# Kernel optimization log

Measured on AMD Instinct MI355X. Metric: run time of the kernel, lower is better.

## Reference

```python
import jax, jax.numpy as jnp
import numpy as np

HEAD_SIZE = 64


def setup_inputs() -> dict:
    key = jax.random.key(0)
    k1, k2, k3, k4 = jax.random.split(key, 4)
    B, T, E = 8, 2048, 1024
    x = jax.random.normal(k1, (B, T, E), dtype=jnp.float32)
    # nn.Linear(n_embd, head_size, bias=False) weights: [head_size, n_embd]
    s = 1.0 / np.sqrt(E)
    Wk = jax.random.uniform(k2, (HEAD_SIZE, E), jnp.float32, -s, s)
    Wq = jax.random.uniform(k3, (HEAD_SIZE, E), jnp.float32, -s, s)
    Wv = jax.random.uniform(k4, (HEAD_SIZE, E), jnp.float32, -s, s)
    return {"x": x, "Wk": Wk, "Wq": Wq, "Wv": Wv}


def reference(x, Wk, Wq, Wv):
    # x: [B, T, E]; W*: [D, E] with D = head_size
    B, T, E = x.shape
    k = jnp.einsum("bte,de->btd", x, Wk)  # [B,T,D]
    q = jnp.einsum("bte,de->btd", x, Wq)
    v = jnp.einsum("bte,de->btd", x, Wv)
    scale = k.shape[-1] ** -0.5
    wei = jnp.einsum("btd,bsd->bts", q, k) * scale  # [B,T,T]
    causal = jnp.tril(jnp.ones((T, T), dtype=bool))
    wei = jnp.where(causal, wei, -jnp.inf)
    wei = jax.nn.softmax(wei, axis=-1)
    # dropout p=0.0 (eval): identity
    return jnp.einsum("bts,bsd->btd", wei, v)
```

## Files before the change

### kernel.cpp

```cpp
#include <hip/hip_runtime.h>
#include <hip/hip_bf16.h>


typedef __bf16 bf16x8 __attribute__((ext_vector_type(8)));
typedef float  f32x4  __attribute__((ext_vector_type(4)));

#define T_SEQ 2048
#define E_DIM 1024
#define D_HEAD 64
#define M_TOT 16384
#define NSPLIT 4
#define SC_LOG2E 0.18033688011112042f

__device__ __forceinline__ unsigned short f2b(float f) {
  union { float f; unsigned int u; } cv; cv.f = f;
  unsigned int u = cv.u;
  u += 0x7FFFu + ((u >> 16) & 1u);
  return (unsigned short)(u >> 16);
}

__device__ __forceinline__ unsigned int f2b2(float a, float b) {
#if __has_builtin(__builtin_amdgcn_cvt_pk_bf16_f32)
  typedef __bf16 bf16x2_t __attribute__((ext_vector_type(2)));
  union { bf16x2_t v; unsigned int u; } cv;
  cv.v = __builtin_amdgcn_cvt_pk_bf16_f32(a, b);
  return cv.u;
#else
  return (unsigned int)f2b(a) | ((unsigned int)f2b(b) << 16);
#endif
}

__device__ __forceinline__ void dma16(const unsigned short* g, unsigned short* l) {
  __builtin_amdgcn_global_load_lds(
      (const __attribute__((address_space(1))) void*)g,
      (__attribute__((address_space(3))) void*)l, 16, 0, 0);
}

__global__ __launch_bounds__(256) void wcvt_kernel(
    const float* __restrict__ Wk, const float* __restrict__ Wq,
    const float* __restrict__ Wv, unsigned short* __restrict__ Wb)
{
  int i = blockIdx.x * 256 + threadIdx.x;
  int n = i >> 8, c4 = i & 255;
  const float* src = (n < 64) ? Wq + n * E_DIM
                   : (n < 128) ? Wk + (n - 64) * E_DIM
                               : Wv + (n - 128) * E_DIM;
  float4 v = *(const float4*)(src + c4 * 4);
  *(uint2*)(Wb + (size_t)n * E_DIM + c4 * 4) = make_uint2(f2b2(v.x, v.y), f2b2(v.z, v.w));
}

__global__ __launch_bounds__(256, 2) void proj_kernel(
    const float* __restrict__ x, const unsigned short* __restrict__ Wb,
    unsigned short* __restrict__ qws, unsigned short* __restrict__ kws,
    unsigned short* __restrict__ vtws)
{
  __shared__ __align__(16) unsigned short x_lds[2][32 * 64];
  __shared__ __align__(16) unsigned short w_lds[2][192 * 64];

  const int tid = threadIdx.x, wv = tid >> 6, lane = tid & 63;
  const int c = lane & 15, quad = lane >> 4;
  const int row0 = blockIdx.x * 32;

  const int f0r = tid >> 4, f0c = tid & 15;
  const int f1r = 16 + f0r;
  const float* xp0 = x + (size_t)(row0 + f0r) * E_DIM + f0c * 4;
  const float* xp1 = x + (size_t)(row0 + f1r) * E_DIM + f0c * 4;
  const int xa0 = f0r * 64 + (((f0c >> 1) ^ (f0r & 7)) << 3) + (f0c & 1) * 4;
  const int xa1 = f1r * 64 + (((f0c >> 1) ^ (f1r & 7)) << 3) + (f0c & 1) * 4;

  auto stageW = [&](int k0, int buf) {
    for (int j = 0; j < 6; ++j) {
      int base_r = (wv * 6 + j) * 8;
      int r = base_r + (lane >> 3);
      int g = (lane & 7) ^ (r & 7);
      dma16(Wb + (size_t)r * E_DIM + k0 + g * 8, &w_lds[buf][base_r * 64]);
    }
  };
  auto writeX = [&](float4 v0, float4 v1, int buf) {
    *(uint2*)&x_lds[buf][xa0] = make_uint2(f2b2(v0.x, v0.y), f2b2(v0.z, v0.w));
    *(uint2*)&x_lds[buf][xa1] = make_uint2(f2b2(v1.x, v1.y), f2b2(v1.z, v1.w));
  };

  f32x4 acc[6];
  for (int j = 0; j < 6; ++j)
    for (int r = 0; r < 4; ++r) acc[j][r] = 0.0f;

  stageW(0, 0);
  {
    float4 v0 = *(const float4*)xp0;
    float4 v1 = *(const float4*)xp1;
    writeX(v0, v1, 0);
  }

  for (int s = 0; s < 16; ++s) {
    const int cur = s & 1;
    __syncthreads();
    float4 v0, v1;
    if (s < 15) {
      const int k1 = (s + 1) * 64;
      stageW(k1, cur ^ 1);
      v0 = *(const float4*)(xp0 + k1);
      v1 = *(const float4*)(xp1 + k1);
    }
    for (int ks = 0; ks < 2; ++ks) {
      const int pg = ((ks * 4 + quad) ^ (c & 7)) << 3;
      bf16x8 a0 = *(const bf16x8*)&x_lds[cur][c * 64 + pg];
      bf16x8 a1 = *(const bf16x8*)&x_lds[cur][(16 + c) * 64 + pg];
      for (int j = 0; j < 3; ++j) {
        const int n = (wv * 3 + j) * 16 + c;
        bf16x8 bb = *(const bf16x8*)&w_lds[cur][n * 64 + pg];
        acc[j * 2]     = __builtin_amdgcn_mfma_f32_16x16x32_bf16(a0, bb, acc[j * 2], 0, 0, 0);
        acc[j * 2 + 1] = __builtin_amdgcn_mfma_f32_16x16x32_bf16(a1, bb, acc[j * 2 + 1], 0, 0, 0);
      }
    }
    if (s < 15) writeX(v0, v1, cur ^ 1);
  }

  for (int mt = 0; mt < 2; ++mt) {
    const int rbase = row0 + mt * 16 + quad * 4;
    for (int j = 0; j < 3; ++j) {
      const int nt = wv * 3 + j;
      const f32x4 a = acc[j * 2 + mt];
      if (nt < 4) {
        int d = nt * 16 + c;
        for (int r = 0; r < 4; ++r)
          qws[(size_t)(rbase + r) * D_HEAD + d] = f2b(a[r] * SC_LOG2E);
      } else if (nt < 8) {
        int d = (nt - 4) * 16 + c;
        for (int r = 0; r < 4; ++r)
          kws[(size_t)(rbase + r) * D_HEAD + d] = f2b(a[r]);
      } else {
        int d = (nt - 8) * 16 + c;
        int bb = rbase >> 11, tt = rbase & 2047;
        *(ushort4*)&vtws[(size_t)bb * D_HEAD * T_SEQ + (size_t)d * T_SEQ + tt] =
            make_ushort4(f2b(a[0]), f2b(a[1]), f2b(a[2]), f2b(a[3]));
      }
    }
  }
}

__global__ __launch_bounds__(256, 4) void attn_kernel(
    const unsigned short* __restrict__ qws, const unsigned short* __restrict__ kws,
    const unsigned short* __restrict__ vtws,
    unsigned short* __restrict__ opart, float* __restrict__ lpart)
{
  __shared__ __align__(16) unsigned short k_lds[2 * 64 * 64];
  __shared__ __align__(16) unsigned short v_lds[2 * 64 * 64];
  __shared__ __align__(16) unsigned short p_lds[64 * 64];

  const int tid = threadIdx.x, wv = tid >> 6, lane = tid & 63;
  const int c = lane & 15, quad = lane >> 4;
  const int qt = blockIdx.x, b = blockIdx.y, sg = blockIdx.z;
  const int t0 = qt * 64;
  const size_t qkb = (size_t)b * T_SEQ * D_HEAD;
  const size_t vtb = (size_t)b * D_HEAD * T_SEQ;
  const int niter = (qt >= sg) ? ((qt - sg) >> 2) + 1 : 0;
  const int rloc = wv * 16 + quad * 4;
  const size_t prow = ((size_t)sg * 8 + b) * T_SEQ;

  if (niter == 0) {
    for (int nt = 0; nt < 4; ++nt)
      for (int r = 0; r < 4; ++r)
        opart[(prow + t0 + rloc + r) * D_HEAD + nt * 16 + c] = 0;
    if (c == 0)
      for (int r = 0; r < 4; ++r) lpart[prow + t0 + rloc + r] = 0.0f;
    return;
  }

  const int mrow = wv * 16 + c;
  const bf16x8 qf0 = *(const bf16x8*)(qws + qkb + (size_t)(t0 + mrow) * D_HEAD + quad * 8);
  const bf16x8 qf1 = *(const bf16x8*)(qws + qkb + (size_t)(t0 + mrow) * D_HEAD + 32 + quad * 8);

  bf16x8 ones;
  { union { unsigned short s[8]; bf16x8 v; } o;
    for (int i = 0; i < 8; ++i) o.s[i] = 0x3F80;
    ones = o.v; }

  f32x4 acc_o[4], acc_l;
  for (int r = 0; r < 4; ++r) acc_l[r] = 0.0f;
  for (int nt = 0; nt < 4; ++nt)
    for (int r = 0; r < 4; ++r) acc_o[nt][r] = 0.0f;

  auto stageKV = [&](int s0, int buf) {
    unsigned short* kb = k_lds + buf * 4096;
    unsigned short* vb = v_lds + buf * 4096;
    for (int j = 0; j < 2; ++j) {
      int base = (wv * 2 + j) * 64;
      int p = base + lane;
      int r = p >> 3, g = (p & 7) ^ (r & 7);
      dma16(kws + qkb + (size_t)(s0 + r) * D_HEAD + g * 8, kb + base * 8);
    }
    for (int j = 0; j < 2; ++j) {
      int base = (wv * 2 + j) * 64;
      int p = base + lane;
      int r = p >> 3, g = (p & 7) ^ (r & 7);
      dma16(vtws + vtb + (size_t)r * T_SEQ + s0 + g * 8, vb + base * 8);
    }
  };

  const bool mydiag = (sg == (qt & 3));
  stageKV(sg * 64, 0);

  for (int it = 0; it < niter; ++it) {
    const int s0 = (sg + 4 * it) * 64;
    const int cur = it & 1;
    __syncthreads();
    if (it + 1 < niter) stageKV((sg + 4 * (it + 1)) * 64, cur ^ 1);

    const unsigned short* kb = k_lds + cur * 4096;
    const unsigned short* vb = v_lds + cur * 4096;

    f32x4 accs[4];
    for (int nt = 0; nt < 4; ++nt)
      for (int r = 0; r < 4; ++r) accs[nt][r] = 0.0f;
    for (int nt = 0; nt < 4; ++nt) {
      int n = nt * 16 + c;
      bf16x8 kf0 = *(const bf16x8*)&kb[n * 64 + ((quad ^ (n & 7)) << 3)];
      bf16x8 kf1 = *(const bf16x8*)&kb[n * 64 + (((4 + quad) ^ (n & 7)) << 3)];
      accs[nt] = __builtin_amdgcn_mfma_f32_16x16x32_bf16(qf0, kf0, accs[nt], 0, 0, 0);
      accs[nt] = __builtin_amdgcn_mfma_f32_16x16x32_bf16(qf1, kf1, accs[nt], 0, 0, 0);
    }
    if (mydiag && it == niter - 1) {
      for (int nt = 0; nt < 4; ++nt) {
        int scol = s0 + nt * 16 + c;
        for (int r = 0; r < 4; ++r)
          if (scol > t0 + rloc + r) accs[nt][r] = -__builtin_inff();
      }
    }

    for (int nt = 0; nt < 4; ++nt)
      for (int r = 0; r < 4; ++r)
        accs[nt][r] = __builtin_exp2f(accs[nt][r]);

    for (int nt = 0; nt < 4; ++nt)
      for (int r = 0; r < 4; ++r) {
        int rr = rloc + r;
        p_lds[rr * 64 + (((nt * 2 + (c >> 3)) ^ (rr & 7)) << 3) + (c & 7)] = f2b(accs[nt][r]);
      }

    for (int ks = 0; ks < 2; ++ks) {
      int kg = ks * 4 + quad;
      bf16x8 pf = *(const bf16x8*)&p_lds[mrow * 64 + ((kg ^ (mrow & 7)) << 3)];
      acc_l = __builtin_amdgcn_mfma_f32_16x16x32_bf16(pf, ones, acc_l, 0, 0, 0);
      for (int nt = 0; nt < 4; ++nt) {
        int n = nt * 16 + c;
        bf16x8 vv = *(const bf16x8*)&vb[n * 64 + ((kg ^ (n & 7)) << 3)];
        acc_o[nt] = __builtin_amdgcn_mfma_f32_16x16x32_bf16(pf, vv, acc_o[nt], 0, 0, 0);
      }
    }
  }

  for (int nt = 0; nt < 4; ++nt)
    for (int r = 0; r < 4; ++r)
      opart[(prow + t0 + rloc + r) * D_HEAD + nt * 16 + c] = f2b(acc_o[nt][r]);
  if (c == 0)
    for (int r = 0; r < 4; ++r) lpart[prow + t0 + rloc + r] = acc_l[r];
}

__global__ __launch_bounds__(256) void merge_kernel(
    const unsigned short* __restrict__ opart, const float* __restrict__ lpart,
    float* __restrict__ out)
{
  int gid = blockIdx.x * 256 + threadIdx.x;
  int gr = gid >> 4, d4 = (gid & 15) * 4;
  float L = 0.0f;
  for (int i = 0; i < NSPLIT; ++i) L += lpart[(size_t)i * M_TOT + gr];
  float inv = 1.0f / L;
  float4 o = make_float4(0.f, 0.f, 0.f, 0.f);
  for (int i = 0; i < NSPLIT; ++i) {
    ushort4 u = *(const ushort4*)(opart + (size_t)i * M_TOT * D_HEAD + (size_t)gr * D_HEAD + d4);
    union { unsigned int u; float f; } cx, cy, cz, cw;
    cx.u = (unsigned int)u.x << 16; cy.u = (unsigned int)u.y << 16;
    cz.u = (unsigned int)u.z << 16; cw.u = (unsigned int)u.w << 16;
    o.x += cx.f; o.y += cy.f; o.z += cz.f; o.w += cw.f;
  }
  o.x *= inv; o.y *= inv; o.z *= inv; o.w *= inv;
  *(float4*)(out + (size_t)gr * D_HEAD + d4) = o;
}

extern "C" void kernel_launch(void* const* d_in, const int* in_sizes, int n_in,
                              void* d_out, int out_size, void* d_ws, size_t ws_size,
                              hipStream_t stream) {
  const float* x  = (const float*)d_in[0];
  const float* Wk = (const float*)d_in[1];
  const float* Wq = (const float*)d_in[2];
  const float* Wv = (const float*)d_in[3];
  float* out = (float*)d_out;

  unsigned short* qws   = (unsigned short*)d_ws;
  unsigned short* kws   = qws + (size_t)M_TOT * D_HEAD;
  unsigned short* vtws  = kws + (size_t)M_TOT * D_HEAD;
  unsigned short* Wb    = vtws + (size_t)M_TOT * D_HEAD;
  unsigned short* opart = Wb + 192 * E_DIM;
  float* lpart = (float*)(opart + (size_t)NSPLIT * M_TOT * D_HEAD);

  wcvt_kernel<<<192, 256, 0, stream>>>(Wk, Wq, Wv, Wb);
  proj_kernel<<<M_TOT / 32, 256, 0, stream>>>(x, Wb, qws, kws, vtws);
  attn_kernel<<<dim3(T_SEQ / 64, 8, NSPLIT), 256, 0, stream>>>(qws, kws, vtws, opart, lpart);
  merge_kernel<<<M_TOT * 16 / 256, 256, 0, stream>>>(opart, lpart, out);
}
```

Baseline: 139.3 us.

## DMA fp32 x tiles to LDS, reverse attention tile order, skip empty splits

```diff
diff --git a/kernel.cpp b/kernel.cpp
--- a/kernel.cpp
+++ b/kernel.cpp
@@ -30,7 +30,7 @@
 #endif
 }
 
-__device__ __forceinline__ void dma16(const unsigned short* g, unsigned short* l) {
+__device__ __forceinline__ void dma16(const void* g, void* l) {
   __builtin_amdgcn_global_load_lds(
       (const __attribute__((address_space(1))) void*)g,
       (__attribute__((address_space(3))) void*)l, 16, 0, 0);
@@ -54,21 +54,20 @@
     unsigned short* __restrict__ qws, unsigned short* __restrict__ kws,
     unsigned short* __restrict__ vtws)
 {
-  __shared__ __align__(16) unsigned short x_lds[2][32 * 64];
+  __shared__ __align__(16) float x_lds[2][32 * 64];
   __shared__ __align__(16) unsigned short w_lds[2][192 * 64];
 
   const int tid = threadIdx.x, wv = tid >> 6, lane = tid & 63;
   const int c = lane & 15, quad = lane >> 4;
   const int row0 = blockIdx.x * 32;
 
-  const int f0r = tid >> 4, f0c = tid & 15;
-  const int f1r = 16 + f0r;
-  const float* xp0 = x + (size_t)(row0 + f0r) * E_DIM + f0c * 4;
-  const float* xp1 = x + (size_t)(row0 + f1r) * E_DIM + f0c * 4;
-  const int xa0 = f0r * 64 + (((f0c >> 1) ^ (f0r & 7)) << 3) + (f0c & 1) * 4;
-  const int xa1 = f1r * 64 + (((f0c >> 1) ^ (f1r & 7)) << 3) + (f0c & 1) * 4;
-
-  auto stageW = [&](int k0, int buf) {
+  auto stage = [&](int k0, int buf) {
+    for (int j = 0; j < 2; ++j) {
+      int base = (wv * 2 + j) * 64;
+      int ci = base + lane;
+      int r = ci >> 4, p = ci & 15, g = p ^ (r & 15);
+      dma16(x + (size_t)(row0 + r) * E_DIM + k0 + g * 4, &x_lds[buf][base * 4]);
+    }
     for (int j = 0; j < 6; ++j) {
       int base_r = (wv * 6 + j) * 8;
       int r = base_r + (lane >> 3);
@@ -76,44 +75,44 @@
       dma16(Wb + (size_t)r * E_DIM + k0 + g * 8, &w_lds[buf][base_r * 64]);
     }
   };
-  auto writeX = [&](float4 v0, float4 v1, int buf) {
-    *(uint2*)&x_lds[buf][xa0] = make_uint2(f2b2(v0.x, v0.y), f2b2(v0.z, v0.w));
-    *(uint2*)&x_lds[buf][xa1] = make_uint2(f2b2(v1.x, v1.y), f2b2(v1.z, v1.w));
-  };
 
   f32x4 acc[6];
   for (int j = 0; j < 6; ++j)
     for (int r = 0; r < 4; ++r) acc[j][r] = 0.0f;
 
-  stageW(0, 0);
-  {
-    float4 v0 = *(const float4*)xp0;
-    float4 v1 = *(const float4*)xp1;
-    writeX(v0, v1, 0);
-  }
+  stage(0, 0);
 
   for (int s = 0; s < 16; ++s) {
     const int cur = s & 1;
     __syncthreads();
-    float4 v0, v1;
-    if (s < 15) {
-      const int k1 = (s + 1) * 64;
-      stageW(k1, cur ^ 1);
-      v0 = *(const float4*)(xp0 + k1);
-      v1 = *(const float4*)(xp1 + k1);
-    }
+    if (s < 15) stage((s + 1) * 64, cur ^ 1);
+
     for (int ks = 0; ks < 2; ++ks) {
+      const int g0 = ks * 8 + quad * 2;
+      union { unsigned int u[4]; bf16x8 v; } A0, A1;
+      {
+        const int m = c;
+        f32x4 v1 = *(const f32x4*)&x_lds[cur][m * 64 + ((g0 ^ (m & 15)) << 2)];
+        f32x4 v2 = *(const f32x4*)&x_lds[cur][m * 64 + (((g0 + 1) ^ (m & 15)) << 2)];
+        A0.u[0] = f2b2(v1[0], v1[1]); A0.u[1] = f2b2(v1[2], v1[3]);
+        A0.u[2] = f2b2(v2[0], v2[1]); A0.u[3] = f2b2(v2[2], v2[3]);
+      }
+      {
+        const int m = 16 + c;
+        f32x4 v1 = *(const f32x4*)&x_lds[cur][m * 64 + ((g0 ^ (m & 15)) << 2)];
+        f32x4 v2 = *(const f32x4*)&x_lds[cur][m * 64 + (((g0 + 1) ^ (m & 15)) << 2)];
+        A1.u[0] = f2b2(v1[0], v1[1]); A1.u[1] = f2b2(v1[2], v1[3]);
+        A1.u[2] = f2b2(v2[0], v2[1]); A1.u[3] = f2b2(v2[2], v2[3]);
+      }
       const int pg = ((ks * 4 + quad) ^ (c & 7)) << 3;
-      bf16x8 a0 = *(const bf16x8*)&x_lds[cur][c * 64 + pg];
-      bf16x8 a1 = *(const bf16x8*)&x_lds[cur][(16 + c) * 64 + pg];
+      (void)pg;
       for (int j = 0; j < 3; ++j) {
         const int n = (wv * 3 + j) * 16 + c;
-        bf16x8 bb = *(const bf16x8*)&w_lds[cur][n * 64 + pg];
-        acc[j * 2]     = __builtin_amdgcn_mfma_f32_16x16x32_bf16(a0, bb, acc[j * 2], 0, 0, 0);
-        acc[j * 2 + 1] = __builtin_amdgcn_mfma_f32_16x16x32_bf16(a1, bb, acc[j * 2 + 1], 0, 0, 0);
-      }
-    }
-    if (s < 15) writeX(v0, v1, cur ^ 1);
+        bf16x8 bb = *(const bf16x8*)&w_lds[cur][n * 64 + (((ks * 4 + quad) ^ (n & 7)) << 3)];
+        acc[j * 2]     = __builtin_amdgcn_mfma_f32_16x16x32_bf16(A0.v, bb, acc[j * 2], 0, 0, 0);
+        acc[j * 2 + 1] = __builtin_amdgcn_mfma_f32_16x16x32_bf16(A1.v, bb, acc[j * 2 + 1], 0, 0, 0);
+      }
+    }
   }
 
   for (int mt = 0; mt < 2; ++mt) {
@@ -150,22 +149,15 @@
 
   const int tid = threadIdx.x, wv = tid >> 6, lane = tid & 63;
   const int c = lane & 15, quad = lane >> 4;
-  const int qt = blockIdx.x, b = blockIdx.y, sg = blockIdx.z;
+  const int qt = 31 - blockIdx.x, b = blockIdx.y, sg = blockIdx.z;
   const int t0 = qt * 64;
   const size_t qkb = (size_t)b * T_SEQ * D_HEAD;
   const size_t vtb = (size_t)b * D_HEAD * T_SEQ;
   const int niter = (qt >= sg) ? ((qt - sg) >> 2) + 1 : 0;
+  if (niter == 0) return;
+
   const int rloc = wv * 16 + quad * 4;
   const size_t prow = ((size_t)sg * 8 + b) * T_SEQ;
-
-  if (niter == 0) {
-    for (int nt = 0; nt < 4; ++nt)
-      for (int r = 0; r < 4; ++r)
-        opart[(prow + t0 + rloc + r) * D_HEAD + nt * 16 + c] = 0;
-    if (c == 0)
-      for (int r = 0; r < 4; ++r) lpart[prow + t0 + rloc + r] = 0.0f;
-    return;
-  }
 
   const int mrow = wv * 16 + c;
   const bf16x8 qf0 = *(const bf16x8*)(qws + qkb + (size_t)(t0 + mrow) * D_HEAD + quad * 8);
@@ -263,17 +255,19 @@
 {
   int gid = blockIdx.x * 256 + threadIdx.x;
   int gr = gid >> 4, d4 = (gid & 15) * 4;
+  const int jmax = (gr & 2047) >> 6;
   float L = 0.0f;
-  for (int i = 0; i < NSPLIT; ++i) L += lpart[(size_t)i * M_TOT + gr];
-  float inv = 1.0f / L;
   float4 o = make_float4(0.f, 0.f, 0.f, 0.f);
   for (int i = 0; i < NSPLIT; ++i) {
+    if (i > jmax) break;
+    L += lpart[(size_t)i * M_TOT + gr];
     ushort4 u = *(const ushort4*)(opart + (size_t)i * M_TOT * D_HEAD + (size_t)gr * D_HEAD + d4);
     union { unsigned int u; float f; } cx, cy, cz, cw;
     cx.u = (unsigned int)u.x << 16; cy.u = (unsigned int)u.y << 16;
     cz.u = (unsigned int)u.z << 16; cw.u = (unsigned int)u.w << 16;
     o.x += cx.f; o.y += cy.f; o.z += cz.f; o.w += cw.f;
   }
+  float inv = 1.0f / L;
   o.x *= inv; o.y *= inv; o.z *= inv; o.w *= inv;
   *(float4*)(out + (size_t)gr * D_HEAD + d4) = o;
 }
@@ -296,6 +290,6 @@
 
   wcvt_kernel<<<192, 256, 0, stream>>>(Wk, Wq, Wv, Wb);
   proj_kernel<<<M_TOT / 32, 256, 0, stream>>>(x, Wb, qws, kws, vtws);
-  attn_kernel<<<dim3(T_SEQ / 64, 8, NSPLIT), 256, 0, stream>>>(qws, kws, vtws, opart, lpart);
+  attn_kernel<<<dim3(32, 8, NSPLIT), 256, 0, stream>>>(qws, kws, vtws, opart, lpart);
   merge_kernel<<<M_TOT * 16 / 256, 256, 0, stream>>>(opart, lpart, out);
 }
```

After: 135.9 us. 2.4% less time.
